# Performance work log

Measured on AMD Instinct MI355X. Metric: run time of the kernel, lower is better.

## Reference

```python
import jax, jax.numpy as jnp
import numpy as np

GROUP_NUM = 4
NODE_NUM = 4096
FEAT_DIM = 128
THRESHOLD = 0.6


def setup_inputs() -> dict:
    key = jax.random.key(0)
    # kaiming-uniform-ish init for the learned bridge-node features
    bound = np.sqrt(6.0 / FEAT_DIM)  # fan_in = feat_dim
    nodes = jax.random.uniform(key, (GROUP_NUM, NODE_NUM, FEAT_DIM),
                               dtype=jnp.float32, minval=-bound, maxval=bound)
    return {"nodes": nodes}


def reference(nodes):
    # Per group g: sim = sigmoid(nodes_g @ nodes_g.T); adj = where(sim < t, 0, sim)
    # [g, n, f] x [g, m, f] -> [g, n, m]
    node_dot = jnp.einsum('gnf,gmf->gnm', nodes, nodes)
    node_sim = jax.nn.sigmoid(node_dot)
    inner_adj = jnp.where(node_sim < THRESHOLD, jnp.zeros((), node_sim.dtype), node_sim)
    # edge_index = inner_adj.nonzero() in the original is data-dependent stream
    # compaction; the dense weighted adjacency carries the same information.
    return inner_adj
```

## Files before the change

### kernel.cpp

```cpp
#include <hip/hip_runtime.h>
#include <math.h>


constexpr int GROUPS = 4;
constexpr int N = 4096;
constexpr int F = 128;
constexpr int BT = 128;
constexpr int TILES = N / BT;
constexpr int PAIRS = TILES * (TILES + 1) / 2;
constexpr float THRESH = 0.6f;
constexpr float LOGIT = 0.405465108f;
constexpr float BAND = 0.006f;

constexpr size_t H_OFF_SHORTS = 8;
constexpr size_t H_ELEMS = (size_t)GROUPS * N * F;

using short8 = __attribute__((ext_vector_type(8))) short;
using f32x4  = __attribute__((ext_vector_type(4))) float;

__device__ __forceinline__ int row_start(int r) { return r * TILES - (r * (r - 1)) / 2; }

__device__ __forceinline__ short f2bf_rne(float x) {
    unsigned u = __float_as_uint(x);
    return (short)((u + 0x7FFFu + ((u >> 16) & 1u)) >> 16);
}

__global__ void split_kernel(const float* __restrict__ in, short* __restrict__ h,
                             unsigned* __restrict__ cnt) {
    const int i = blockIdx.x * 256 + threadIdx.x;
    if (i == 0) *cnt = 0;
    if (i < (int)H_ELEMS) h[i] = f2bf_rne(in[i]);
}

#define GLL16(gp, lp)                                                        \
    __builtin_amdgcn_global_load_lds(                                        \
        (const __attribute__((address_space(1))) void*)(gp),                 \
        (__attribute__((address_space(3))) void*)(lp), 16, 0, 0)

__global__ __launch_bounds__(256, 2)
void bridge_mfma_kernel(const short* __restrict__ W, float* __restrict__ out,
                        unsigned* __restrict__ cnt, unsigned* __restrict__ list,
                        unsigned cap) {
    __shared__ alignas(16) short ldsA[BT * F];
    __shared__ alignas(16) short ldsB[BT * F];

    const int g = blockIdx.y;
    const int t = blockIdx.x;
    int bm = (int)((2 * TILES + 1
                    - sqrtf((float)((2 * TILES + 1) * (2 * TILES + 1) - 8 * t))) * 0.5f);
    bm = bm < 0 ? 0 : (bm > TILES - 1 ? TILES - 1 : bm);
    while (row_start(bm) > t) --bm;
    while (row_start(bm + 1) <= t) ++bm;
    const int bn = bm + (t - row_start(bm));

    const int tid  = threadIdx.x;
    const int lane = tid & 63;
    const int wv   = tid >> 6;
    const int lm   = lane & 15;
    const int q    = lane >> 4;
    const int R    = (wv & 1) * 64;
    const int C    = (wv >> 1) * 64;

    const short* baseA = W + ((size_t)g * N + bm * BT) * F;
    const short* baseB = W + ((size_t)g * N + bn * BT) * F;

#pragma unroll
    for (int it = 0; it < 8; ++it) {
        const int g0 = tid + 256 * it;
        const int r  = g0 >> 4;
        const int o  = g0 & 15;
        const int so = o ^ (r & 15);
        GLL16(baseA + (size_t)r * F + so * 8, &ldsA[g0 * 8]);
        GLL16(baseB + (size_t)r * F + so * 8, &ldsB[g0 * 8]);
    }
    __syncthreads();

    f32x4 acc[4][4] = {};
#pragma unroll
    for (int kc = 0; kc < 4; ++kc) {
        short8 af[4], bf[4];
#pragma unroll
        for (int i = 0; i < 4; ++i) {
            const int row = R + i * 16 + lm;
            af[i] = *(const short8*)(ldsA + row * 16 * 8 + (((kc * 4 + q) ^ lm) * 8));
        }
#pragma unroll
        for (int j = 0; j < 4; ++j) {
            const int row = C + j * 16 + lm;
            bf[j] = *(const short8*)(ldsB + row * 16 * 8 + (((kc * 4 + q) ^ lm) * 8));
        }
#pragma unroll
        for (int i = 0; i < 4; ++i)
#pragma unroll
            for (int j = 0; j < 4; ++j)
                acc[i][j] = __builtin_amdgcn_mfma_f32_16x16x32_bf16(
                    af[i], bf[j], acc[i][j], 0, 0, 0);
    }

    __syncthreads();
    unsigned* sc = (unsigned*)ldsA;
    if (tid == 0) sc[0] = 0;

    float val[4][4][4];
    unsigned local[8];
    int nf = 0;
#pragma unroll
    for (int i = 0; i < 4; ++i)
#pragma unroll
        for (int j = 0; j < 4; ++j)
#pragma unroll
            for (int r = 0; r < 4; ++r) {
                const float x = acc[i][j][r];
                const float e = __expf(-x);
                const float s = __builtin_amdgcn_rcpf(1.0f + e);
                val[i][j][r] = (s < THRESH) ? 0.0f : s;
                if (fabsf(x - LOGIT) < BAND) {
                    const unsigned row = bm * BT + R + i * 16 + q * 4 + r;
                    const unsigned col = bn * BT + C + j * 16 + lm;
                    const unsigned enc = ((unsigned)g << 24) | (row << 12) | col;
                    if (nf < 8) local[nf++] = enc;
                    else {
                        const unsigned idx = atomicAdd(cnt, 1u);
                        if (idx < cap) list[idx] = enc;
                    }
                }
            }

    const size_t outg = (size_t)g * N * N;

#pragma unroll
    for (int i = 0; i < 4; ++i)
#pragma unroll
        for (int r = 0; r < 4; ++r) {
            const int row = bm * BT + R + i * 16 + q * 4 + r;
            float* o = out + outg + (size_t)row * N + bn * BT + C;
#pragma unroll
            for (int j = 0; j < 4; ++j)
                o[j * 16 + lm] = val[i][j][r];
        }

    if (bm != bn) {
#pragma unroll
        for (int j = 0; j < 4; ++j) {
            const int mrow = bn * BT + C + j * 16 + lm;
            float* o = out + outg + (size_t)mrow * N + bm * BT + R;
#pragma unroll
            for (int i = 0; i < 4; ++i) {
                float4 v = {val[i][j][0], val[i][j][1], val[i][j][2], val[i][j][3]};
                *(float4*)(o + i * 16 + q * 4) = v;
            }
        }
    }

    __syncthreads();
    unsigned myoff = 0;
    if (nf) myoff = atomicAdd(&sc[0], (unsigned)nf);
    __syncthreads();
    if (tid == 0) sc[1] = sc[0] ? atomicAdd(cnt, sc[0]) : 0u;
    __syncthreads();
    if (nf) {
        const unsigned base = sc[1] + myoff;
        for (int k = 0; k < nf; ++k)
            if (base + k < cap) list[base + k] = local[k];
    }
}

__global__ void fixup_kernel(const float* __restrict__ nodes, float* __restrict__ out,
                             const unsigned* __restrict__ cnt,
                             const unsigned* __restrict__ list, unsigned cap) {
    unsigned n = *cnt;
    if (n > cap) n = cap;
    const unsigned stride = gridDim.x * blockDim.x;
    for (unsigned idx = blockIdx.x * blockDim.x + threadIdx.x; idx < n; idx += stride) {
        const unsigned p = list[idx];
        const unsigned g = p >> 24, row = (p >> 12) & 0xFFF, col = p & 0xFFF;
        const float* a = nodes + ((size_t)g * N + row) * F;
        const float* b = nodes + ((size_t)g * N + col) * F;
        float acc = 0.0f;
        for (int k = 0; k < F; ++k)
            acc = fmaf(a[k], b[k], acc);
        const float s = 1.0f / (1.0f + expf(-acc));
        const float v = (s < THRESH) ? 0.0f : s;
        out[(size_t)g * N * N + (size_t)row * N + col] = v;
        out[(size_t)g * N * N + (size_t)col * N + row] = v;
    }
}

extern "C" void kernel_launch(void* const* d_in, const int* in_sizes, int n_in,
                              void* d_out, int out_size, void* d_ws, size_t ws_size,
                              hipStream_t stream) {
    const float* nodes = (const float*)d_in[0];
    float* out = (float*)d_out;

    unsigned* cnt = (unsigned*)d_ws;
    short* h = (short*)d_ws + H_OFF_SHORTS;
    const size_t list_off_bytes = 16 + H_ELEMS * sizeof(short);
    unsigned* list = (unsigned*)((char*)d_ws + list_off_bytes);
    const size_t cap_sz = (ws_size > list_off_bytes + 16)
                              ? (ws_size - list_off_bytes) / sizeof(unsigned) : 0;
    const unsigned cap = (unsigned)(cap_sz > (1u << 22) ? (1u << 22) : cap_sz);

    split_kernel<<<(int)((H_ELEMS + 255) / 256), 256, 0, stream>>>(nodes, h, cnt);

    dim3 grid(PAIRS, GROUPS);
    bridge_mfma_kernel<<<grid, 256, 0, stream>>>(h, out, cnt, list, cap);

    fixup_kernel<<<512, 256, 0, stream>>>(nodes, out, cnt, list, cap);
}
```

Measured before the change: 332.6 us.

## Compute full tile grid with halved LDS and transposed-only float4 stores

Drops the triangular symmetric tiling and instead launches all 32x32 tile pairs per group. Each block writes only the transposed, float4-vectorized output. K is split into two 64-wide halves, which halves LDS per block and lets launch bounds ask for 4 blocks per CU. This removes the scalar strided stores and the register-heavy val array to raise occupancy, at the cost of doing the GEMM and sigmoid work roughly twice and adding a barrier between K halves. Fixup records now use the transposed coordinates.

```diff
diff --git a/kernel.cpp b/kernel.cpp
--- a/kernel.cpp
+++ b/kernel.cpp
@@ -7,7 +7,6 @@
 constexpr int F = 128;
 constexpr int BT = 128;
 constexpr int TILES = N / BT;
-constexpr int PAIRS = TILES * (TILES + 1) / 2;
 constexpr float THRESH = 0.6f;
 constexpr float LOGIT = 0.405465108f;
 constexpr float BAND = 0.006f;
@@ -17,8 +16,6 @@
 
 using short8 = __attribute__((ext_vector_type(8))) short;
 using f32x4  = __attribute__((ext_vector_type(4))) float;
-
-__device__ __forceinline__ int row_start(int r) { return r * TILES - (r * (r - 1)) / 2; }
 
 __device__ __forceinline__ short f2bf_rne(float x) {
     unsigned u = __float_as_uint(x);
@@ -37,21 +34,16 @@
         (const __attribute__((address_space(1))) void*)(gp),                 \
         (__attribute__((address_space(3))) void*)(lp), 16, 0, 0)
 
-__global__ __launch_bounds__(256, 2)
+__global__ __launch_bounds__(256, 4)
 void bridge_mfma_kernel(const short* __restrict__ W, float* __restrict__ out,
                         unsigned* __restrict__ cnt, unsigned* __restrict__ list,
                         unsigned cap) {
-    __shared__ alignas(16) short ldsA[BT * F];
-    __shared__ alignas(16) short ldsB[BT * F];
+    __shared__ alignas(16) short ldsA[BT * 64];
+    __shared__ alignas(16) short ldsB[BT * 64];
 
-    const int g = blockIdx.y;
-    const int t = blockIdx.x;
-    int bm = (int)((2 * TILES + 1
-                    - sqrtf((float)((2 * TILES + 1) * (2 * TILES + 1) - 8 * t))) * 0.5f);
-    bm = bm < 0 ? 0 : (bm > TILES - 1 ? TILES - 1 : bm);
-    while (row_start(bm) > t) --bm;
-    while (row_start(bm + 1) <= t) ++bm;
-    const int bn = bm + (t - row_start(bm));
+    const int g  = blockIdx.y;
+    const int bm = blockIdx.x >> 5;
+    const int bn = blockIdx.x & 31;
 
     const int tid  = threadIdx.x;
     const int lane = tid & 63;
@@ -64,60 +56,70 @@
     const short* baseA = W + ((size_t)g * N + bm * BT) * F;
     const short* baseB = W + ((size_t)g * N + bn * BT) * F;
 
+    f32x4 acc[4][4] = {};
+
 #pragma unroll
-    for (int it = 0; it < 8; ++it) {
-        const int g0 = tid + 256 * it;
-        const int r  = g0 >> 4;
-        const int o  = g0 & 15;
-        const int so = o ^ (r & 15);
-        GLL16(baseA + (size_t)r * F + so * 8, &ldsA[g0 * 8]);
-        GLL16(baseB + (size_t)r * F + so * 8, &ldsB[g0 * 8]);
-    }
-    __syncthreads();
+    for (int kh = 0; kh < 2; ++kh) {
+        if (kh) __syncthreads();
+        const int ko = kh * 64;
+#pragma unroll
+        for (int it = 0; it < 4; ++it) {
+            const int g0 = tid + 256 * it;
+            const int r  = g0 >> 3;
+            const int o  = g0 & 7;
+            const int so = o ^ (r & 7);
+            GLL16(baseA + (size_t)r * F + ko + so * 8, &ldsA[g0 * 8]);
+            GLL16(baseB + (size_t)r * F + ko + so * 8, &ldsB[g0 * 8]);
+        }
+        __syncthreads();
 
-    f32x4 acc[4][4] = {};
 #pragma unroll
-    for (int kc = 0; kc < 4; ++kc) {
-        short8 af[4], bf[4];
+        for (int kcl = 0; kcl < 2; ++kcl) {
+            const int oc = kcl * 4 + q;
+            short8 af[4], bf[4];
 #pragma unroll
-        for (int i = 0; i < 4; ++i) {
-            const int row = R + i * 16 + lm;
-            af[i] = *(const short8*)(ldsA + row * 16 * 8 + (((kc * 4 + q) ^ lm) * 8));
+            for (int i = 0; i < 4; ++i) {
+                const int row = R + i * 16 + lm;
+                af[i] = *(const short8*)(ldsA + row * 64 + ((oc ^ (lm & 7)) * 8));
+            }
+#pragma unroll
+            for (int j = 0; j < 4; ++j) {
+                const int row = C + j * 16 + lm;
+                bf[j] = *(const short8*)(ldsB + row * 64 + ((oc ^ (lm & 7)) * 8));
+            }
+#pragma unroll
+            for (int i = 0; i < 4; ++i)
+#pragma unroll
+                for (int j = 0; j < 4; ++j)
+                    acc[i][j] = __builtin_amdgcn_mfma_f32_16x16x32_bf16(
+                        af[i], bf[j], acc[i][j], 0, 0, 0);
         }
-#pragma unroll
-        for (int j = 0; j < 4; ++j) {
-            const int row = C + j * 16 + lm;
-            bf[j] = *(const short8*)(ldsB + row * 16 * 8 + (((kc * 4 + q) ^ lm) * 8));
-        }
-#pragma unroll
-        for (int i = 0; i < 4; ++i)
-#pragma unroll
-            for (int j = 0; j < 4; ++j)
-                acc[i][j] = __builtin_amdgcn_mfma_f32_16x16x32_bf16(
-                    af[i], bf[j], acc[i][j], 0, 0, 0);
     }
 
     __syncthreads();
     unsigned* sc = (unsigned*)ldsA;
     if (tid == 0) sc[0] = 0;
+    __syncthreads();
 
-    float val[4][4][4];
+    const size_t outg = (size_t)g * N * N;
     unsigned local[8];
     int nf = 0;
 #pragma unroll
-    for (int i = 0; i < 4; ++i)
+    for (int j = 0; j < 4; ++j) {
+        const unsigned orow = bn * BT + C + j * 16 + lm;
+        float* o = out + outg + (size_t)orow * N + bm * BT + R;
+        float v[4][4];
 #pragma unroll
-        for (int j = 0; j < 4; ++j)
+        for (int i = 0; i < 4; ++i)
 #pragma unroll
             for (int r = 0; r < 4; ++r) {
                 const float x = acc[i][j][r];
                 const float e = __expf(-x);
                 const float s = __builtin_amdgcn_rcpf(1.0f + e);
-                val[i][j][r] = (s < THRESH) ? 0.0f : s;
+                v[i][r] = (s < THRESH) ? 0.0f : s;
                 if (fabsf(x - LOGIT) < BAND) {
-                    const unsigned row = bm * BT + R + i * 16 + q * 4 + r;
-                    const unsigned col = bn * BT + C + j * 16 + lm;
-                    const unsigned enc = ((unsigned)g << 24) | (row << 12) | col;
+                    const unsigned ocol = bm * BT + R + i * 16 + q * 4 + r;
+                    const unsigned enc = ((unsigned)g << 24) | (orow << 12) | ocol;
                     if (nf < 8) local[nf++] = enc;
                     else {
                         const unsigned idx = atomicAdd(cnt, 1u);
@@ -125,30 +127,10 @@
                     }
                 }
             }
-
-    const size_t outg = (size_t)g * N * N;
-
 #pragma unroll
-    for (int i = 0; i < 4; ++i)
-#pragma unroll
-        for (int r = 0; r < 4; ++r) {
-            const int row = bm * BT + R + i * 16 + q * 4 + r;
-            float* o = out + outg + (size_t)row * N + bn * BT + C;
-#pragma unroll
-            for (int j = 0; j < 4; ++j)
-                o[j * 16 + lm] = val[i][j][r];
-        }
-
-    if (bm != bn) {
-#pragma unroll
-        for (int j = 0; j < 4; ++j) {
-            const int mrow = bn * BT + C + j * 16 + lm;
-            float* o = out + outg + (size_t)mrow * N + bm * BT + R;
-#pragma unroll
-            for (int i = 0; i < 4; ++i) {
-                float4 v = {val[i][j][0], val[i][j][1], val[i][j][2], val[i][j][3]};
-                *(float4*)(o + i * 16 + q * 4) = v;
-            }
+        for (int i = 0; i < 4; ++i) {
+            float4 t = {v[i][0], v[i][1], v[i][2], v[i][3]};
+            *(float4*)(o + i * 16 + q * 4) = t;
         }
     }
 
@@ -202,7 +184,7 @@
 
     split_kernel<<<(int)((H_ELEMS + 255) / 256), 256, 0, stream>>>(nodes, h, cnt);
 
-    dim3 grid(PAIRS, GROUPS);
+    dim3 grid(TILES * TILES, GROUPS);
     bridge_mfma_kernel<<<grid, 256, 0, stream>>>(h, out, cnt, list, cap);
 
     fixup_kernel<<<512, 256, 0, stream>>>(nodes, out, cnt, list, cap);
```

Measured after the change: 337.8 us. No clear change (+1.6%).
